# Kernel optimization log

Hardware: AMD Instinct MI355X
Metric: run time of the kernel (lower is better)

## Reference

```python
import jax, jax.numpy as jnp
from jax import lax
import numpy as np

B, C, H, W = 8, 192, 128, 128
HEADS, WS, SS = 6, 8, 4
HID = 768  # 4 * C
HEAD_DIM = C // HEADS
SCALE = HEAD_DIM ** -0.5
EPS = 1e-5


def _rel_pos_index(ws):
    coords = np.stack(np.meshgrid(np.arange(ws), np.arange(ws), indexing='ij'))  # (2, ws, ws)
    flat = coords.reshape(2, ws * ws)
    rel = flat[:, :, None] - flat[:, None, :]          # (2, N, N)
    rel = rel.transpose(1, 2, 0)                       # (N, N, 2)
    rel[:, :, 0] += ws - 1
    rel[:, :, 1] += ws - 1
    rel[:, :, 0] *= 2 * ws - 1
    return rel.sum(-1).astype(np.int32)                # (N, N)


def _attn_mask(hp, wp, ws, ss):
    # Swin shift mask: 0 where tokens share a region, -100 otherwise. (nW, N, N)
    img = np.zeros((hp, wp), dtype=np.float32)
    slices = (slice(0, -ws), slice(-ws, -ss), slice(-ss, None))
    cnt = 0
    for hs in slices:
        for ws_ in slices:
            img[hs, ws_] = float(cnt)
            cnt += 1
    mw = img.reshape(hp // ws, ws, wp // ws, ws).transpose(0, 2, 1, 3).reshape(-1, ws * ws)
    am = mw[:, None, :] - mw[:, :, None]
    return np.where(am != 0, -100.0, 0.0).astype(np.float32)


def _layernorm(x, g, b):
    mu = jnp.mean(x, axis=-1, keepdims=True)
    var = jnp.mean(jnp.square(x - mu), axis=-1, keepdims=True)
    return (x - mu) * lax.rsqrt(var + EPS) * g + b


def setup_inputs() -> dict:
    key = jax.random.key(0)
    ks = jax.random.split(key, 16)
    s = 0.02
    return {
        'x': jax.random.normal(ks[0], (B, C, H, W), jnp.float32),
        'pos_conv_w': jax.random.normal(ks[1], (C, 1, 3, 3), jnp.float32) * s,
        'norm1_g': jnp.ones((C,), jnp.float32),
        'norm1_b': jnp.zeros((C,), jnp.float32),
        'qkv_w': jax.random.normal(ks[2], (C, 3 * C), jnp.float32) * s,
        'qkv_b': jnp.zeros((3 * C,), jnp.float32),
        'proj_w': jax.random.normal(ks[3], (C, C), jnp.float32) * s,
        'proj_b': jnp.zeros((C,), jnp.float32),
        'rel_bias_table': jax.random.normal(ks[4], ((2 * WS - 1) ** 2, HEADS), jnp.float32) * s,
        'norm2_g': jnp.ones((C,), jnp.float32),
        'norm2_b': jnp.zeros((C,), jnp.float32),
        'mlp_w1': jax.random.normal(ks[5], (C, HID), jnp.float32) * s,
        'mlp_b1': jnp.zeros((HID,), jnp.float32),
        'mlp_w2': jax.random.normal(ks[6], (HID, C), jnp.float32) * s,
        'mlp_b2': jnp.zeros((C,), jnp.float32),
    }


def reference(x, pos_conv_w, norm1_g, norm1_b, qkv_w, qkv_b, proj_w, proj_b,
              rel_bias_table, norm2_g, norm2_b, mlp_w1, mlp_b1, mlp_w2, mlp_b2):
    b, c, h, w = x.shape
    ws, ss, nh, hd = WS, SS, HEADS, HEAD_DIM
    N = ws * ws

    # depthwise 3x3 positional conv (residual)
    x = x + lax.conv_general_dilated(
        x, pos_conv_w, (1, 1), 'SAME', feature_group_count=c,
        dimension_numbers=('NCHW', 'OIHW', 'NCHW'))

    if ss > 0:
        x = jnp.roll(x, (-ss, -ss), axis=(2, 3))

    pad_h = (ws - h % ws) % ws
    pad_w = (ws - w % ws) % ws
    if pad_h or pad_w:
        x = jnp.pad(x, ((0, 0), (0, 0), (0, pad_h), (0, pad_w)))
    hp, wp = h + pad_h, w + pad_w

    # window partition -> (num_windows, N, c)
    windows = x.reshape(b, c, hp // ws, ws, wp // ws, ws)
    windows = windows.transpose(0, 2, 4, 3, 5, 1).reshape(-1, N, c)
    nw = windows.shape[0]

    a = _layernorm(windows, norm1_g, norm1_b)
    qkv = (a @ qkv_w + qkv_b).reshape(nw, N, 3, nh, hd).transpose(2, 0, 3, 1, 4)
    q, k, v = qkv[0], qkv[1], qkv[2]                      # (nw, nh, N, hd)

    attn = jnp.einsum('whnd,whmd->whnm', q * SCALE, k)    # (nw, nh, N, N)

    rel_idx = jnp.asarray(_rel_pos_index(ws))             # (N, N) int
    bias = rel_bias_table[rel_idx.reshape(-1)].reshape(N, N, nh).transpose(2, 0, 1)
    attn = attn + bias[None]

    if ss > 0:
        mask = jnp.asarray(_attn_mask(hp, wp, ws, ss))    # (nW_per_img, N, N)
        nwpb = (hp // ws) * (wp // ws)
        attn = attn.reshape(b, nwpb, nh, N, N) + mask[None, :, None]
        attn = attn.reshape(nw, nh, N, N)

    attn = jax.nn.softmax(attn, axis=-1)
    out = jnp.einsum('whnm,whmd->whnd', attn, v).transpose(0, 2, 1, 3).reshape(nw, N, c)

    windows = windows + out @ proj_w + proj_b
    hmid = jax.nn.gelu(_layernorm(windows, norm2_g, norm2_b) @ mlp_w1 + mlp_b1, approximate=False)
    windows = windows + hmid @ mlp_w2 + mlp_b2

    # unpartition -> (b, c, hp, wp), crop, roll back
    y = windows.reshape(b, hp // ws, wp // ws, ws, ws, c)
    y = y.transpose(0, 5, 1, 3, 2, 4).reshape(b, c, hp, wp)[:, :, :h, :w]
    if ss > 0:
        y = jnp.roll(y, (ss, ss), axis=(2, 3))
    return y
```

## Files before the change

kernel.cpp:

```cpp
#include <hip/hip_runtime.h>
#include <hip/hip_bf16.h>
#include <cstdint>
#include <cstddef>

typedef short short8 __attribute__((ext_vector_type(8)));
typedef float float4_ __attribute__((ext_vector_type(4)));
typedef unsigned int uint4_ __attribute__((ext_vector_type(4)));
typedef unsigned int uint2_ __attribute__((ext_vector_type(2)));

#define DEVI static __device__ __forceinline__

DEVI unsigned short f2bf(float f) {
  union { float f; unsigned u; } v; v.f = f;
  return (unsigned short)((v.u + 0x7FFFu + ((v.u >> 16) & 1u)) >> 16);
}
DEVI unsigned pack2bf(float a, float b) {
  return (unsigned)f2bf(a) | ((unsigned)f2bf(b) << 16);
}
DEVI unsigned short f2bfc(float f) {
  __hip_bfloat16 h = __float2bfloat16(f);
  union { __hip_bfloat16 h1; unsigned short u; } cv; cv.h1 = h; return cv.u;
}
DEVI unsigned pack2bfc(float a, float b) {
  float2 f2; f2.x = a; f2.y = b;
  __hip_bfloat162 h = __float22bfloat162_rn(f2);
  union { __hip_bfloat162 h2; unsigned u; } cv; cv.h2 = h; return cv.u;
}
DEVI float bf2f(unsigned short h) {
  union { unsigned u; float f; } v; v.u = ((unsigned)h) << 16;
  return v.f;
}
DEVI float gelu_f(float x) {
  float u = x * (0.7978845608f + 0.0356774081f * x * x);
  float e = exp2f(-2.8853900818f * u);
  return x * __builtin_amdgcn_rcpf(1.0f + e);
}

#define SCALE_Q 0.17677669529663687f

__global__ __launch_bounds__(256) void k_prep(
    const float* __restrict__ qkv_w, const float* __restrict__ qkv_b,
    const float* __restrict__ proj_w, const float* __restrict__ mlp_w1,
    const float* __restrict__ mlp_w2, const float* __restrict__ relt,
    unsigned short* __restrict__ qkvWT, unsigned short* __restrict__ projWT,
    unsigned short* __restrict__ w1T, unsigned short* __restrict__ w2T,
    float* __restrict__ qkv_b_s, float* __restrict__ bias_attn) {
  int i = blockIdx.x * 256 + threadIdx.x;
  if (i < 110592) { int n = i / 192, k = i - n * 192;
    float v = qkv_w[k * 576 + n]; if (n < 192) v *= SCALE_Q;
    qkvWT[i] = f2bf(v); return; }
  i -= 110592;
  if (i < 576) { qkv_b_s[i] = qkv_b[i] * (i < 192 ? SCALE_Q : 1.0f); return; }
  i -= 576;
  if (i < 36864) { int n = i / 192, k = i - n * 192;
    projWT[i] = f2bf(proj_w[k * 192 + n]); return; }
  i -= 36864;
  if (i < 147456) { int n = i / 192, k = i - n * 192;
    w1T[i] = f2bf(mlp_w1[k * 768 + n]); return; }
  i -= 147456;
  if (i < 147456) { int n = i / 768, k = i - n * 768;
    w2T[i] = f2bf(mlp_w2[k * 192 + n]); return; }
  i -= 147456;
  if (i < 24576) {
    int h = i >> 12, nm = i & 4095, n = nm >> 6, m = nm & 63;
    int dr = (n >> 3) - (m >> 3) + 7, dc = (n & 7) - (m & 7) + 7;
    bias_attn[i] = relt[(dr * 15 + dc) * 6 + h];
  }
}

__global__ __launch_bounds__(256) void k_conv(
    const float* __restrict__ x, const float* __restrict__ convw,
    unsigned short* __restrict__ temp) {
  __shared__ float s_in[66 * 128];
  int bx = blockIdx.x;
  int c = bx >> 1, seg = bx & 1, b = blockIdx.y;
  int h0 = seg * 64;
  int t = threadIdx.x;
  const float* xp = x + ((size_t)(b * 192 + c)) * 16384;
  #pragma unroll
  for (int i = 0; i < 9; ++i) {
    int q = t + i * 256;
    if (q < 2112) {
      int srow = q >> 5, chunk = q & 31;
      float4_ v = *(const float4_*)(xp + ((h0 + 3 + srow) & 127) * 128 + chunk * 4);
      *(float4_*)(s_in + srow * 128 + chunk * 4) = v;
    }
  }
  float cw9[9];
  #pragma unroll
  for (int i = 0; i < 9; ++i) cw9[i] = convw[c * 9 + i];
  __syncthreads();
  int r2 = t >> 7;
  int wp = t & 127;
  int w_true = (wp + 4) & 127;
  float mw0 = (w_true != 0) ? 1.f : 0.f;
  float mw2 = (w_true != 127) ? 1.f : 0.f;
  int wl0 = (w_true + 127) & 127, wl2 = (w_true + 1) & 127;
  unsigned short* tp = temp + ((size_t)(b * 192 + c)) * 16384;
  #pragma unroll 4
  for (int it = 0; it < 32; ++it) {
    int r = it * 2 + r2;
    int h_true = (h0 + 4 + r) & 127;
    float mh0 = (h_true != 0) ? 1.f : 0.f;
    float mh2 = (h_true != 127) ? 1.f : 0.f;
    const float* row0 = s_in + r * 128;
    const float* row1 = row0 + 128;
    const float* row2 = row1 + 128;
    float acc = row1[w_true];
    acc = fmaf(cw9[0], mh0 * mw0 * row0[wl0], acc);
    acc = fmaf(cw9[1], mh0 * row0[w_true], acc);
    acc = fmaf(cw9[2], mh0 * mw2 * row0[wl2], acc);
    acc = fmaf(cw9[3], mw0 * row1[wl0], acc);
    acc = fmaf(cw9[4], row1[w_true], acc);
    acc = fmaf(cw9[5], mw2 * row1[wl2], acc);
    acc = fmaf(cw9[6], mh2 * mw0 * row2[wl0], acc);
    acc = fmaf(cw9[7], mh2 * row2[w_true], acc);
    acc = fmaf(cw9[8], mh2 * mw2 * row2[wl2], acc);
    tp[(size_t)(h0 + r) * 128 + wp] = f2bf(acc);
  }
}

__global__ __launch_bounds__(256) void k_lnw(
    const unsigned short* __restrict__ temp, const float* __restrict__ g1,
    const float* __restrict__ b1, unsigned short* __restrict__ xw,
    unsigned short* __restrict__ a) {
  __shared__ unsigned short sT[192 * 128];
  __shared__ float s_g[192], s_b[192];
  int t = threadIdx.x;
  for (int i = t; i < 192; i += 256) { s_g[i] = g1[i]; s_b[i] = b1[i]; }
  int wj0 = blockIdx.x * 2, wi = blockIdx.y, b = blockIdx.z;
  const unsigned short* tb = temp + (size_t)b * (192 * 16384) + (wi * 8) * 128 + wj0 * 8;
  #pragma unroll
  for (int i = 0; i < 12; ++i) {
    int id = t + i * 256;
    int c = id >> 4, rem = id & 15, r = rem >> 1, piece = rem & 1;
    short8 v = *(const short8*)(tb + (size_t)c * 16384 + r * 128 + piece * 8);
    *(short8*)(sT + c * 128 + piece * 64 + r * 8) = v;
  }
  __syncthreads();
  int tok = t >> 1, half = t & 1, c0 = half * 96;
  size_t gtok = ((size_t)(b * 256 + wi * 16 + wj0 + (tok >> 6))) * 64 + (tok & 63);
  unsigned short* xwp = xw + gtok * 192 + c0;
  float sum = 0.f, sq = 0.f;
  #pragma unroll
  for (int j8 = 0; j8 < 12; ++j8) {
    unsigned short raw[8];
    unsigned pk[4];
    #pragma unroll
    for (int e = 0; e < 8; ++e) {
      unsigned short rv = sT[(c0 + j8 * 8 + e) * 128 + tok];
      raw[e] = rv;
      float x = bf2f(rv);
      sum += x; sq = fmaf(x, x, sq);
    }
    #pragma unroll
    for (int k = 0; k < 4; ++k) pk[k] = (unsigned)raw[2 * k] | ((unsigned)raw[2 * k + 1] << 16);
    uint4_ pv = { pk[0], pk[1], pk[2], pk[3] };
    *(uint4_*)(xwp + j8 * 8) = pv;
  }
  sum += __shfl_xor(sum, 1);
  sq  += __shfl_xor(sq, 1);
  float mu = sum * (1.f / 192.f);
  float var = sq * (1.f / 192.f) - mu * mu;
  float rs = rsqrtf(var + 1e-5f);
  unsigned short* ap = a + gtok * 192 + c0;
  #pragma unroll
  for (int j8 = 0; j8 < 12; ++j8) {
    unsigned pk[4];
    #pragma unroll
    for (int k = 0; k < 4; ++k) {
      int c = c0 + j8 * 8 + k * 2;
      float v0 = (bf2f(sT[c * 128 + tok]) - mu) * rs * s_g[c] + s_b[c];
      float v1 = (bf2f(sT[(c + 1) * 128 + tok]) - mu) * rs * s_g[c + 1] + s_b[c + 1];
      pk[k] = pack2bf(v0, v1);
    }
    uint4_ pv = { pk[0], pk[1], pk[2], pk[3] };
    *(uint4_*)(ap + j8 * 8) = pv;
  }
}

__global__ __launch_bounds__(384, 1) void k_qkvattn(
    const unsigned short* __restrict__ a, const unsigned short* __restrict__ wT,
    const float* __restrict__ qbias, const float* __restrict__ biasAll,
    unsigned short* __restrict__ outO) {
  __shared__ __align__(16) unsigned short sQK[6][4096];
  __shared__ __align__(16) unsigned short sVT[6][2048];
  int t = threadIdx.x, lane = t & 63, head = t / 64;
  int win = blockIdx.x;
  int wi = (win >> 4) & 15, wj = win & 15;
  int lrow = lane & 15, lkgrp = lane >> 4, lk = lkgrp * 8;
  const unsigned short* aWin = a + (size_t)win * (64 * 192);
  char* qk = (char*)sQK[head];
  char* vt = (char*)sVT[head];

  auto gemmQKV = [&](int sel) {
    const unsigned short* wb = wT + (size_t)(sel * 192 + head * 32) * 192;
    const float* bb = qbias + sel * 192 + head * 32;
    short8 bw[2][6];
    #pragma unroll
    for (int nb = 0; nb < 2; ++nb)
      #pragma unroll
      for (int ks = 0; ks < 6; ++ks)
        bw[nb][ks] = *(const short8*)(wb + (size_t)(nb * 16 + lrow) * 192 + ks * 32 + lk);
    float4_ acc[2][4];
    #pragma unroll
    for (int nb = 0; nb < 2; ++nb)
      #pragma unroll
      for (int mi = 0; mi < 4; ++mi) acc[nb][mi] = (float4_){0.f, 0.f, 0.f, 0.f};
    short8 af0[4], af1[4];
    #pragma unroll
    for (int mi = 0; mi < 4; ++mi)
      af0[mi] = *(const short8*)(aWin + (size_t)(mi * 16 + lrow) * 192 + lk);
    #pragma unroll
    for (int mi = 0; mi < 4; ++mi)
      af1[mi] = *(const short8*)(aWin + (size_t)(mi * 16 + lrow) * 192 + 32 + lk);
    #pragma unroll
    for (int ks = 0; ks < 6; ++ks) {
      #pragma unroll
      for (int mi = 0; mi < 4; ++mi) {
        short8 a_ = (ks & 1) ? af1[mi] : af0[mi];
        #pragma unroll
        for (int nb = 0; nb < 2; ++nb)
          acc[nb][mi] = __builtin_amdgcn_mfma_f32_16x16x32_bf16(a_, bw[nb][ks], acc[nb][mi], 0, 0, 0);
      }
      if (ks < 4) {
        #pragma unroll
        for (int mi = 0; mi < 4; ++mi) {
          short8 nv = *(const short8*)(aWin + (size_t)(mi * 16 + lrow) * 192 + (ks + 2) * 32 + lk);
          if (ks & 1) af1[mi] = nv; else af0[mi] = nv;
        }
      }
    }
    #pragma unroll
    for (int nb = 0; nb < 2; ++nb) {
      float bv = bb[nb * 16 + lrow];
      int d = nb * 16 + lrow;
      #pragma unroll
      for (int mi = 0; mi < 4; ++mi)
        #pragma unroll
        for (int e = 0; e < 4; ++e) {
          unsigned short pv = f2bfc(acc[nb][mi][e] + bv);
          int tok = mi * 16 + lkgrp * 4 + e;
          if (sel == 2)
            *(unsigned short*)(vt + ((d * 128 + tok * 2) ^ ((d & 7) << 4))) = pv;
          else
            *(unsigned short*)(qk + sel * 4096 + ((tok * 64 + d * 2) ^ ((tok & 7) << 4))) = pv;
        }
    }
  };
  gemmQKV(0);
  gemmQKV(1);
  gemmQKV(2);

  short8 kf[4];
  #pragma unroll
  for (int ni = 0; ni < 4; ++ni) {
    int tokk = ni * 16 + lrow;
    kf[ni] = *(const short8*)(qk + 4096 + ((tokk * 64 + lk * 2) ^ ((tokk & 7) << 4)));
  }
  float4_ s[4][4];
  #pragma unroll
  for (int mi = 0; mi < 4; ++mi) {
    int tokq = mi * 16 + lrow;
    short8 qf = *(const short8*)(qk + ((tokq * 64 + lk * 2) ^ ((tokq & 7) << 4)));
    #pragma unroll
    for (int ni = 0; ni < 4; ++ni) {
      s[mi][ni] = (float4_){0.f, 0.f, 0.f, 0.f};
      s[mi][ni] = __builtin_amdgcn_mfma_f32_16x16x32_bf16(qf, kf[ni], s[mi][ni], 0, 0, 0);
    }
  }
  const float* bh = biasAll + head * 4096;
  bool wi15 = (wi == 15), wj15 = (wj == 15);
  bool edge = wi15 || wj15;
  #pragma unroll
  for (int mi = 0; mi < 4; ++mi) {
    #pragma unroll
    for (int e = 0; e < 4; ++e) {
      int row = mi * 16 + lkgrp * 4 + e;
      int rcls = (wi15 ? ((row >> 3) >= 4 ? 2 : 1) : 0) * 3 +
                 (wj15 ? ((row & 7) >= 4 ? 2 : 1) : 0);
      float v[4];
      #pragma unroll
      for (int ni = 0; ni < 4; ++ni) {
        int col = ni * 16 + lrow;
        float xv = s[mi][ni][e] + bh[row * 64 + col];
        if (edge) {
          int ccls = (wi15 ? ((col >> 3) >= 4 ? 2 : 1) : 0) * 3 +
                     (wj15 ? ((col & 7) >= 4 ? 2 : 1) : 0);
          if (ccls != rcls) xv -= 100.f;
        }
        v[ni] = xv;
      }
      float mx = fmaxf(fmaxf(v[0], v[1]), fmaxf(v[2], v[3]));
      mx = fmaxf(mx, __shfl_xor(mx, 1));
      mx = fmaxf(mx, __shfl_xor(mx, 2));
      mx = fmaxf(mx, __shfl_xor(mx, 4));
      mx = fmaxf(mx, __shfl_xor(mx, 8));
      float sm = 0.f;
      #pragma unroll
      for (int ni = 0; ni < 4; ++ni) { v[ni] = __expf(v[ni] - mx); sm += v[ni]; }
      sm += __shfl_xor(sm, 1);
      sm += __shfl_xor(sm, 2);
      sm += __shfl_xor(sm, 4);
      sm += __shfl_xor(sm, 8);
      float inv = 1.f / sm;
      #pragma unroll
      for (int ni = 0; ni < 4; ++ni) {
        int col = ni * 16 + lrow;
        *(unsigned short*)(qk + ((row * 128 + col * 2) ^ ((row & 7) << 4))) = f2bfc(v[ni] * inv);
      }
    }
  }
  float4_ o[2][4];
  #pragma unroll
  for (int db = 0; db < 2; ++db)
    #pragma unroll
    for (int qb2 = 0; qb2 < 4; ++qb2) o[db][qb2] = (float4_){0.f, 0.f, 0.f, 0.f};
  #pragma unroll
  for (int kk = 0; kk < 2; ++kk) {
    int ktok = kk * 32 + lk;
    short8 vf[2], pf[4];
    #pragma unroll
    for (int db = 0; db < 2; ++db) {
      int d = db * 16 + lrow;
      vf[db] = *(const short8*)(vt + ((d * 128 + ktok * 2) ^ ((d & 7) << 4)));
    }
    #pragma unroll
    for (int qb2 = 0; qb2 < 4; ++qb2) {
      int rq = qb2 * 16 + lrow;
      pf[qb2] = *(const short8*)(qk + ((rq * 128 + ktok * 2) ^ ((rq & 7) << 4)));
    }
    #pragma unroll
    for (int db = 0; db < 2; ++db)
      #pragma unroll
      for (int qb2 = 0; qb2 < 4; ++qb2)
        o[db][qb2] = __builtin_amdgcn_mfma_f32_16x16x32_bf16(vf[db], pf[qb2], o[db][qb2], 0, 0, 0);
  }
  unsigned short* ob = outO + (size_t)win * (64 * 192);
  #pragma unroll
  for (int qb2 = 0; qb2 < 4; ++qb2)
    #pragma unroll
    for (int db = 0; db < 2; ++db) {
      unsigned lo = pack2bfc(o[db][qb2][0], o[db][qb2][1]);
      unsigned hi = pack2bfc(o[db][qb2][2], o[db][qb2][3]);
      uint2_ pv = { lo, hi };
      *(uint2_*)(ob + (size_t)(qb2 * 16 + lrow) * 192 + head * 32 + db * 16 + lkgrp * 4) = pv;
    }
}

__global__ __launch_bounds__(256, 2) void k_mlp(
    const unsigned short* __restrict__ O, const unsigned short* __restrict__ xw,
    const unsigned short* __restrict__ projWT, const float* __restrict__ proj_b,
    const float* __restrict__ n2g, const float* __restrict__ n2b,
    const unsigned short* __restrict__ w1T, const float* __restrict__ mlpb1,
    const unsigned short* __restrict__ w2T, const float* __restrict__ mlpb2,
    float* __restrict__ y) {
  __shared__ __align__(16) unsigned short sH[64 * 192];
  __shared__ __align__(16) unsigned short sB2[64 * 192];
  __shared__ float sRed[64 * 8];
  __shared__ unsigned sTok[64];
  int t = threadIdx.x, lane = t & 63, wn = t >> 6;
  int lrow = lane & 15, lkgrp = lane >> 4, lk = lkgrp * 8;
  int blk = blockIdx.x;
  int b = blk >> 8, rem = blk & 255, ta = rem >> 3, tb_ = rem & 7;
  if (t < 64) {
    int rr = t >> 4, ss = t & 15;
    int h = ta * 4 + rr, w = tb_ * 16 + ss;
    int hp = (h + 124) & 127, wp = (w + 124) & 127;
    unsigned gtok = ((unsigned)(b * 256 + (hp >> 3) * 16 + (wp >> 3))) * 64 +
                    (hp & 7) * 8 + (wp & 7);
    sTok[t] = gtok * 192u;
  }
  __syncthreads();
  unsigned aoff[4];
  #pragma unroll
  for (int mi = 0; mi < 4; ++mi) aoff[mi] = sTok[mi * 16 + lrow];
  float4_ tacc[4][3];
  #pragma unroll
  for (int mi = 0; mi < 4; ++mi)
    #pragma unroll
    for (int ni = 0; ni < 3; ++ni) tacc[mi][ni] = (float4_){0.f, 0.f, 0.f, 0.f};
  {
    short8 bP0[3][3], bP1[3][3], af0[4], af1[4];
    #pragma unroll
    for (int ni = 0; ni < 3; ++ni)
      #pragma unroll
      for (int k3 = 0; k3 < 3; ++k3)
        bP0[ni][k3] = *(const short8*)(projWT + (size_t)(wn * 48 + ni * 16 + lrow) * 192 + k3 * 32 + lk);
    #pragma unroll
    for (int mi = 0; mi < 4; ++mi)
      af0[mi] = *(const short8*)(O + aoff[mi] + lk);
    #pragma unroll
    for (int ni = 0; ni < 3; ++ni)
      #pragma unroll
      for (int k3 = 0; k3 < 3; ++k3)
        bP1[ni][k3] = *(const short8*)(projWT + (size_t)(wn * 48 + ni * 16 + lrow) * 192 + (3 + k3) * 32 + lk);
    #pragma unroll
    for (int mi = 0; mi < 4; ++mi)
      af1[mi] = *(const short8*)(O + aoff[mi] + 32 + lk);
    #pragma unroll
    for (int ks = 0; ks < 6; ++ks) {
      #pragma unroll
      for (int mi = 0; mi < 4; ++mi) {
        short8 a_ = (ks & 1) ? af1[mi] : af0[mi];
        #pragma unroll
        for (int ni = 0; ni < 3; ++ni) {
          short8 b_ = (ks < 3) ? bP0[ni][ks] : bP1[ni][ks - 3];
          tacc[mi][ni] = __builtin_amdgcn_mfma_f32_16x16x32_bf16(a_, b_, tacc[mi][ni], 0, 0, 0);
        }
      }
      if (ks < 4) {
        #pragma unroll
        for (int mi = 0; mi < 4; ++mi) {
          short8 nv = *(const short8*)(O + aoff[mi] + (ks + 2) * 32 + lk);
          if (ks & 1) af1[mi] = nv; else af0[mi] = nv;
        }
      }
    }
  }
  {
    unsigned roff[4][4];
    #pragma unroll
    for (int mi = 0; mi < 4; ++mi)
      #pragma unroll
      for (int e = 0; e < 4; ++e)
        roff[mi][e] = sTok[mi * 16 + lkgrp * 4 + e];
    unsigned short rxv[3][4][4];
    #pragma unroll
    for (int ni = 0; ni < 3; ++ni) {
      int col = wn * 48 + ni * 16 + lrow;
      #pragma unroll
      for (int mi = 0; mi < 4; ++mi)
        #pragma unroll
        for (int e = 0; e < 4; ++e)
          rxv[ni][mi][e] = xw[roff[mi][e] + col];
    }
    #pragma unroll
    for (int ni = 0; ni < 3; ++ni) {
      float pbv = proj_b[wn * 48 + ni * 16 + lrow];
      #pragma unroll
      for (int mi = 0; mi < 4; ++mi)
        #pragma unroll
        for (int e = 0; e < 4; ++e)
          tacc[mi][ni][e] += pbv + bf2f(rxv[ni][mi][e]);
    }
  }
  #pragma unroll
  for (int mi = 0; mi < 4; ++mi)
    #pragma unroll
    for (int e = 0; e < 4; ++e) {
      float s1 = tacc[mi][0][e] + tacc[mi][1][e] + tacc[mi][2][e];
      float s2 = tacc[mi][0][e] * tacc[mi][0][e] + tacc[mi][1][e] * tacc[mi][1][e] +
                 tacc[mi][2][e] * tacc[mi][2][e];
      s1 += __shfl_xor(s1, 1); s1 += __shfl_xor(s1, 2); s1 += __shfl_xor(s1, 4); s1 += __shfl_xor(s1, 8);
      s2 += __shfl_xor(s2, 1); s2 += __shfl_xor(s2, 2); s2 += __shfl_xor(s2, 4); s2 += __shfl_xor(s2, 8);
      if (lrow == 0) {
        int row = mi * 16 + lkgrp * 4 + e;
        sRed[row * 8 + wn * 2 + 0] = s1;
        sRed[row * 8 + wn * 2 + 1] = s2;
      }
    }
  __syncthreads();
  #pragma unroll
  for (int mi = 0; mi < 4; ++mi)
    #pragma unroll
    for (int e = 0; e < 4; ++e) {
      int row = mi * 16 + lkgrp * 4 + e;
      float s1 = sRed[row * 8] + sRed[row * 8 + 2] + sRed[row * 8 + 4] + sRed[row * 8 + 6];
      float s2 = sRed[row * 8 + 1] + sRed[row * 8 + 3] + sRed[row * 8 + 5] + sRed[row * 8 + 7];
      float mu = s1 * (1.f / 192.f);
      float var = s2 * (1.f / 192.f) - mu * mu;
      float rs = rsqrtf(var + 1e-5f);
      #pragma unroll
      for (int ni = 0; ni < 3; ++ni) {
        int col = wn * 48 + ni * 16 + lrow;
        float hv = (tacc[mi][ni][e] - mu) * rs * n2g[col] + n2b[col];
        *(unsigned short*)((char*)sH + ((row * 384 + col * 2) ^ ((row & 7) << 4))) = f2bfc(hv);
      }
    }
  __syncthreads();
  short8 bwA[6], bwB[6];
  #pragma unroll
  for (int ks = 0; ks < 6; ++ks)
    bwA[ks] = *(const short8*)(w1T + (size_t)(wn * 48 + lrow) * 192 + ks * 32 + lk);
  #pragma unroll 1
  for (int ch = 0; ch < 4; ++ch) {
    #pragma unroll 1
    for (int ni = 0; ni < 3; ++ni) {
      int nni = (ni < 2) ? ni + 1 : 0;
      int nch = (ni < 2) ? ch : ch + 1;
      if (nch < 4) {
        int gn = nch * 192 + wn * 48 + nni * 16 + lrow;
        #pragma unroll
        for (int ks = 0; ks < 6; ++ks)
          bwB[ks] = *(const short8*)(w1T + (size_t)gn * 192 + ks * 32 + lk);
      }
      float4_ h1[4];
      #pragma unroll
      for (int mi = 0; mi < 4; ++mi) h1[mi] = (float4_){0.f, 0.f, 0.f, 0.f};
      #pragma unroll
      for (int ks = 0; ks < 6; ++ks) {
        int kb = ks * 32 + lk;
        #pragma unroll
        for (int mi = 0; mi < 4; ++mi) {
          int row = mi * 16 + lrow;
          short8 afv = *(const short8*)((const char*)sH + ((row * 384 + kb * 2) ^ ((row & 7) << 4)));
          h1[mi] = __builtin_amdgcn_mfma_f32_16x16x32_bf16(afv, bwA[ks], h1[mi], 0, 0, 0);
        }
      }
      float b1v = mlpb1[ch * 192 + wn * 48 + ni * 16 + lrow];
      int col = wn * 48 + ni * 16 + lrow;
      #pragma unroll
      for (int mi = 0; mi < 4; ++mi)
        #pragma unroll
        for (int e = 0; e < 4; ++e) {
          float v = gelu_f(h1[mi][e] + b1v);
          int row = mi * 16 + lkgrp * 4 + e;
          *(unsigned short*)((char*)sB2 + ((row * 384 + col * 2) ^ ((row & 7) << 4))) = f2bfc(v);
        }
      #pragma unroll
      for (int ks = 0; ks < 6; ++ks) bwA[ks] = bwB[ks];
    }
    short8 cw0[3][3], cw1[3][3];
    #pragma unroll
    for (int ni = 0; ni < 3; ++ni)
      #pragma unroll
      for (int k3 = 0; k3 < 3; ++k3)
        cw0[ni][k3] = *(const short8*)(w2T + (size_t)(wn * 48 + ni * 16 + lrow) * 768 + ch * 192 + k3 * 32 + lk);
    __syncthreads();
    #pragma unroll
    for (int ni = 0; ni < 3; ++ni)
      #pragma unroll
      for (int k3 = 0; k3 < 3; ++k3)
        cw1[ni][k3] = *(const short8*)(w2T + (size_t)(wn * 48 + ni * 16 + lrow) * 768 + ch * 192 + (3 + k3) * 32 + lk);
    #pragma unroll
    for (int ks = 0; ks < 6; ++ks) {
      int kb = ks * 32 + lk;
      short8 af[4];
      #pragma unroll
      for (int mi = 0; mi < 4; ++mi) {
        int row = mi * 16 + lrow;
        af[mi] = *(const short8*)((const char*)sB2 + ((row * 384 + kb * 2) ^ ((row & 7) << 4)));
      }
      #pragma unroll
      for (int mi = 0; mi < 4; ++mi)
        #pragma unroll
        for (int ni = 0; ni < 3; ++ni) {
          short8 b_ = (ks < 3) ? cw0[ni][ks] : cw1[ni][ks - 3];
          tacc[mi][ni] = __builtin_amdgcn_mfma_f32_16x16x32_bf16(af[mi], b_, tacc[mi][ni], 0, 0, 0);
        }
    }
    __syncthreads();
  }
  int wcol = tb_ * 16 + lkgrp * 4;
  #pragma unroll
  for (int ni = 0; ni < 3; ++ni) {
    int col = wn * 48 + ni * 16 + lrow;
    float b2v = mlpb2[col];
    #pragma unroll
    for (int mi = 0; mi < 4; ++mi) {
      int h = ta * 4 + mi;
      float4_ vv;
      #pragma unroll
      for (int e = 0; e < 4; ++e) vv[e] = tacc[mi][ni][e] + b2v;
      *(float4_*)(y + ((size_t)(b * 192 + col) * 128 + h) * 128 + wcol) = vv;
    }
  }
}

extern "C" void kernel_launch(void* const* d_in, const int* in_sizes, int n_in,
                              void* d_out, int out_size, void* d_ws, size_t ws_size,
                              hipStream_t stream) {
  (void)in_sizes; (void)n_in; (void)out_size;
  const float* x    = (const float*)d_in[0];
  const float* pcw  = (const float*)d_in[1];
  const float* n1g  = (const float*)d_in[2];
  const float* n1b  = (const float*)d_in[3];
  const float* qkvw = (const float*)d_in[4];
  const float* qkvb = (const float*)d_in[5];
  const float* pw   = (const float*)d_in[6];
  const float* pb   = (const float*)d_in[7];
  const float* relt = (const float*)d_in[8];
  const float* n2g  = (const float*)d_in[9];
  const float* n2b  = (const float*)d_in[10];
  const float* w1   = (const float*)d_in[11];
  const float* mb1  = (const float*)d_in[12];
  const float* w2   = (const float*)d_in[13];
  const float* mb2  = (const float*)d_in[14];
  float* y = (float*)d_out;
  char* ws = (char*)d_ws;
  size_t off = 0;
  auto carve = [&](size_t bytes) { void* p = ws + off; off += (bytes + 255) & ~(size_t)255; return p; };
  unsigned short* qkvWT  = (unsigned short*)carve(576 * 192 * 2);
  unsigned short* projWT = (unsigned short*)carve(192 * 192 * 2);
  unsigned short* w1T    = (unsigned short*)carve(768 * 192 * 2);
  unsigned short* w2T    = (unsigned short*)carve(192 * 768 * 2);
  float* qkv_b_s   = (float*)carve(576 * 4);
  float* bias_attn = (float*)carve(6 * 64 * 64 * 4);
  unsigned short* aBuf   = (unsigned short*)carve((size_t)131072 * 192 * 2);
  unsigned short* xwBuf  = (unsigned short*)carve((size_t)131072 * 192 * 2);
  unsigned short* temp   = (unsigned short*)carve((size_t)131072 * 192 * 2);
  if (off > ws_size) return;

  k_prep<<<dim3(1827), dim3(256), 0, stream>>>(qkvw, qkvb, pw, w1, w2, relt,
                                               qkvWT, projWT, w1T, w2T, qkv_b_s, bias_attn);
  k_conv<<<dim3(384, 8), dim3(256), 0, stream>>>(x, pcw, temp);
  k_lnw<<<dim3(8, 16, 8), dim3(256), 0, stream>>>(temp, n1g, n1b, xwBuf, aBuf);
  k_qkvattn<<<dim3(2048), dim3(384), 0, stream>>>(aBuf, qkvWT, qkv_b_s, bias_attn, temp);
  k_mlp<<<dim3(2048), dim3(256), 0, stream>>>(temp, xwBuf, projWT, pb, n2g, n2b,
                                              w1T, mb1, w2T, mb2, y);
}
```

Before: 498.9 us.

## Swap MFMA operands for vectorized LDS stores and add setprio around MFMA loops

Swaps the A/B operands of the MFMA in the QKV and MLP-fc1 GEMMs so each lane's four accumulator elements run along the feature dimension instead of the token dimension. Q/K and GELU outputs can then be packed and written to LDS as 8-byte vector stores instead of scalar 2-byte stores, and the bias becomes one float4 load. It also wraps MFMA-heavy loops in s_setprio(1)/s_setprio(0) to favour matrix-issuing waves. The V-transpose path still uses scalar stores, and the priority hints may not help with only a few waves per SIMD.

Result: faster. 487.1 us (-2.4%).

```diff
diff --git a/kernel.cpp b/kernel.cpp
--- a/kernel.cpp
+++ b/kernel.cpp
@@ -221,7 +221,7 @@
         short8 a_ = (ks & 1) ? af1[mi] : af0[mi];
         #pragma unroll
         for (int nb = 0; nb < 2; ++nb)
-          acc[nb][mi] = __builtin_amdgcn_mfma_f32_16x16x32_bf16(a_, bw[nb][ks], acc[nb][mi], 0, 0, 0);
+          acc[nb][mi] = __builtin_amdgcn_mfma_f32_16x16x32_bf16(bw[nb][ks], a_, acc[nb][mi], 0, 0, 0);
       }
       if (ks < 4) {
         #pragma unroll
@@ -233,19 +233,28 @@
     }
     #pragma unroll
     for (int nb = 0; nb < 2; ++nb) {
-      float bv = bb[nb * 16 + lrow];
-      int d = nb * 16 + lrow;
-      #pragma unroll
-      for (int mi = 0; mi < 4; ++mi)
-        #pragma unroll
-        for (int e = 0; e < 4; ++e) {
-          unsigned short pv = f2bfc(acc[nb][mi][e] + bv);
-          int tok = mi * 16 + lkgrp * 4 + e;
-          if (sel == 2)
-            *(unsigned short*)(vt + ((d * 128 + tok * 2) ^ ((d & 7) << 4))) = pv;
-          else
-            *(unsigned short*)(qk + sel * 4096 + ((tok * 64 + d * 2) ^ ((tok & 7) << 4))) = pv;
-        }
+      float4_ b4 = *(const float4_*)(bb + nb * 16 + lkgrp * 4);
+      if (sel == 2) {
+        #pragma unroll
+        for (int mi = 0; mi < 4; ++mi) {
+          int tok = mi * 16 + lrow;
+          #pragma unroll
+          for (int e = 0; e < 4; ++e) {
+            int d = nb * 16 + lkgrp * 4 + e;
+            *(unsigned short*)(vt + ((d * 128 + tok * 2) ^ ((d & 7) << 4))) =
+                f2bfc(acc[nb][mi][e] + b4[e]);
+          }
+        }
+      } else {
+        int dsub2 = (nb * 16 + lkgrp * 4) * 2;
+        #pragma unroll
+        for (int mi = 0; mi < 4; ++mi) {
+          int tok = mi * 16 + lrow;
+          uint2_ pv = { pack2bfc(acc[nb][mi][0] + b4[0], acc[nb][mi][1] + b4[1]),
+                        pack2bfc(acc[nb][mi][2] + b4[2], acc[nb][mi][3] + b4[3]) };
+          *(uint2_*)(qk + sel * 4096 + ((tok * 64 + dsub2) ^ ((tok & 7) << 4))) = pv;
+        }
+      }
     }
   };
   gemmQKV(0);
@@ -259,6 +268,7 @@
     kf[ni] = *(const short8*)(qk + 4096 + ((tokk * 64 + lk * 2) ^ ((tokk & 7) << 4)));
   }
   float4_ s[4][4];
+  __builtin_amdgcn_s_setprio(1);
   #pragma unroll
   for (int mi = 0; mi < 4; ++mi) {
     int tokq = mi * 16 + lrow;
@@ -269,6 +279,7 @@
       s[mi][ni] = __builtin_amdgcn_mfma_f32_16x16x32_bf16(qf, kf[ni], s[mi][ni], 0, 0, 0);
     }
   }
+  __builtin_amdgcn_s_setprio(0);
   const float* bh = biasAll + head * 4096;
   bool wi15 = (wi == 15), wj15 = (wj == 15);
   bool edge = wi15 || wj15;
@@ -316,6 +327,7 @@
   for (int db = 0; db < 2; ++db)
     #pragma unroll
     for (int qb2 = 0; qb2 < 4; ++qb2) o[db][qb2] = (float4_){0.f, 0.f, 0.f, 0.f};
+  __builtin_amdgcn_s_setprio(1);
   #pragma unroll
   for (int kk = 0; kk < 2; ++kk) {
     int ktok = kk * 32 + lk;
@@ -336,6 +348,7 @@
       for (int qb2 = 0; qb2 < 4; ++qb2)
         o[db][qb2] = __builtin_amdgcn_mfma_f32_16x16x32_bf16(vf[db], pf[qb2], o[db][qb2], 0, 0, 0);
   }
+  __builtin_amdgcn_s_setprio(0);
   unsigned short* ob = outO + (size_t)win * (64 * 192);
   #pragma unroll
   for (int qb2 = 0; qb2 < 4; ++qb2)
@@ -498,6 +511,7 @@
       float4_ h1[4];
       #pragma unroll
       for (int mi = 0; mi < 4; ++mi) h1[mi] = (float4_){0.f, 0.f, 0.f, 0.f};
+      __builtin_amdgcn_s_setprio(1);
       #pragma unroll
       for (int ks = 0; ks < 6; ++ks) {
         int kb = ks * 32 + lk;
@@ -505,19 +519,22 @@
         for (int mi = 0; mi < 4; ++mi) {
           int row = mi * 16 + lrow;
           short8 afv = *(const short8*)((const char*)sH + ((row * 384 + kb * 2) ^ ((row & 7) << 4)));
-          h1[mi] = __builtin_amdgcn_mfma_f32_16x16x32_bf16(afv, bwA[ks], h1[mi], 0, 0, 0);
-        }
-      }
-      float b1v = mlpb1[ch * 192 + wn * 48 + ni * 16 + lrow];
-      int col = wn * 48 + ni * 16 + lrow;
-      #pragma unroll
-      for (int mi = 0; mi < 4; ++mi)
-        #pragma unroll
-        for (int e = 0; e < 4; ++e) {
-          float v = gelu_f(h1[mi][e] + b1v);
-          int row = mi * 16 + lkgrp * 4 + e;
-          *(unsigned short*)((char*)sB2 + ((row * 384 + col * 2) ^ ((row & 7) << 4))) = f2bfc(v);
-        }
+          h1[mi] = __builtin_amdgcn_mfma_f32_16x16x32_bf16(bwA[ks], afv, h1[mi], 0, 0, 0);
+        }
+      }
+      __builtin_amdgcn_s_setprio(0);
+      float4_ b4 = *(const float4_*)(mlpb1 + ch * 192 + wn * 48 + ni * 16 + lkgrp * 4);
+      int nsub2 = (wn * 48 + ni * 16 + lkgrp * 4) * 2;
+      #pragma unroll
+      for (int mi = 0; mi < 4; ++mi) {
+        int tok_ = mi * 16 + lrow;
+        float g0 = gelu_f(h1[mi][0] + b4[0]);
+        float g1 = gelu_f(h1[mi][1] + b4[1]);
+        float g2 = gelu_f(h1[mi][2] + b4[2]);
+        float g3 = gelu_f(h1[mi][3] + b4[3]);
+        uint2_ pv = { pack2bfc(g0, g1), pack2bfc(g2, g3) };
+        *(uint2_*)((char*)sB2 + ((tok_ * 384 + nsub2) ^ ((tok_ & 7) << 4))) = pv;
+      }
       #pragma unroll
       for (int ks = 0; ks < 6; ++ks) bwA[ks] = bwB[ks];
     }
@@ -533,6 +550,7 @@
       #pragma unroll
       for (int k3 = 0; k3 < 3; ++k3)
         cw1[ni][k3] = *(const short8*)(w2T + (size_t)(wn * 48 + ni * 16 + lrow) * 768 + ch * 192 + (3 + k3) * 32 + lk);
+    __builtin_amdgcn_s_setprio(1);
     #pragma unroll
     for (int ks = 0; ks < 6; ++ks) {
       int kb = ks * 32 + lk;
@@ -550,6 +568,7 @@
           tacc[mi][ni] = __builtin_amdgcn_mfma_f32_16x16x32_bf16(af[mi], b_, tacc[mi][ni], 0, 0, 0);
         }
     }
+    __builtin_amdgcn_s_setprio(0);
     __syncthreads();
   }
   int wcol = tb_ * 16 + lkgrp * 4;
```
